# Kernel optimization log

Hardware: AMD Instinct MI355X
Metric: run time of the kernel (lower is better)

The kernel has to match this reference:

```python
import jax, jax.numpy as jnp
from jax import lax
import numpy as np

B, N, C, T = 64, 25, 128, 256
EPS = 1e-5


def setup_inputs() -> dict:
    key = jax.random.key(0)
    ks = jax.random.split(key, 4)
    x = jax.random.normal(ks[0], (B, N, C, T), dtype=jnp.float32)
    adj = jax.random.uniform(ks[1], (N, N), dtype=jnp.float32)
    # row-normalize adjacency like a typical GCN propagation matrix
    adj = adj / jnp.sum(adj, axis=1, keepdims=True)
    # xavier-uniform-ish linear weight [out, in]
    lim = float(np.sqrt(6.0 / (C + C)))
    W_gcn = jax.random.uniform(ks[2], (C, C), minval=-lim, maxval=lim, dtype=jnp.float32)
    b_gcn = jnp.zeros((C,), jnp.float32)
    W_conv = jax.random.normal(ks[3], (C, C, 3), dtype=jnp.float32) * (1.0 / np.sqrt(3 * C))
    b_conv = jnp.zeros((C,), jnp.float32)
    return dict(
        x=x, adj=adj, W_gcn=W_gcn, b_gcn=b_gcn, W_conv=W_conv, b_conv=b_conv,
        tc_gamma=jnp.ones((C,), jnp.float32), tc_beta=jnp.zeros((C,), jnp.float32),
        tc_mean=jnp.zeros((C,), jnp.float32), tc_var=jnp.ones((C,), jnp.float32),
        bn_gamma=jnp.ones((C,), jnp.float32), bn_beta=jnp.zeros((C,), jnp.float32),
        bn_mean=jnp.zeros((C,), jnp.float32), bn_var=jnp.ones((C,), jnp.float32),
    )


def _bn(x, gamma, beta, mean, var, axis):
    # eval-mode batchnorm over channel `axis`
    shape = [1] * x.ndim
    shape[axis] = -1
    g = gamma.reshape(shape)
    b = beta.reshape(shape)
    m = mean.reshape(shape)
    v = var.reshape(shape)
    return g * (x - m) * lax.rsqrt(v + EPS) + b


def reference(x, adj, W_gcn, b_gcn, W_conv, b_conv,
              tc_gamma, tc_beta, tc_mean, tc_var,
              bn_gamma, bn_beta, bn_mean, bn_var):
    # x: [B, N, C, T]; in_channels == out_channels so residual is identity
    b_, n_, c_, t_ = x.shape
    residual = x
    # spatial GCN for all timesteps at once: linear over feature dim, then adj matmul over nodes
    h = jnp.einsum('bnct,oc->bnot', x, W_gcn) + b_gcn[None, None, :, None]
    h = jnp.einsum('mn,bnot->bmot', adj, h)  # [B, N, C, T]
    # temporal conv1d over T for every (batch, node) pair at once
    hc = h.reshape(b_ * n_, c_, t_)
    y = lax.conv_general_dilated(hc, W_conv, window_strides=(1,), padding=[(1, 1)],
                                 dimension_numbers=('NCH', 'OIH', 'NCH'))
    y = y + b_conv[None, :, None]
    y = _bn(y, tc_gamma, tc_beta, tc_mean, tc_var, axis=1)
    y = jax.nn.relu(y)
    y = y.reshape(b_, n_, c_, t_)
    # residual add, block batchnorm over channels, relu
    y = y + residual
    y = _bn(y, bn_gamma, bn_beta, bn_mean, bn_var, axis=2)
    y = jax.nn.relu(y)
    return y
```

## Files before the change

kernel.cpp:

```cpp
#include <hip/hip_runtime.h>
#include <hip/hip_bf16.h>
#include <stdint.h>

#define Bn 64
#define Nn 25
#define Cn 128
#define Tn 256
#define EPSC 1e-5f

typedef short bf16x8 __attribute__((ext_vector_type(8)));
typedef float f32x4 __attribute__((ext_vector_type(4)));
typedef int   i32x4 __attribute__((ext_vector_type(4)));

static constexpr size_t X2T_BYTES  = (size_t)Bn * Nn * Tn * Cn * 2;
static constexpr size_t WEFF_OFF   = X2T_BYTES;
static constexpr size_t WEFF_BYTES = (size_t)3 * 128 * 128 * 2;
static constexpr size_t EPI_OFF    = WEFF_OFF + WEFF_BYTES;
static constexpr size_t ROWSUM_OFF = EPI_OFF + (size_t)7 * 128 * 4;
static constexpr size_t ZPAGE_OFF  = ROWSUM_OFF + 256;
static constexpr size_t WS_NEEDED  = ZPAGE_OFF + 256;

__device__ __forceinline__ uint16_t f2bf(float f) {
    uint32_t u = __builtin_bit_cast(uint32_t, f);
    u = (u + 0x7FFFu + ((u >> 16) & 1u)) >> 16;
    return (uint16_t)u;
}

__device__ __forceinline__ void dma16(const void* gsrc, void* ldst) {
    __builtin_amdgcn_global_load_lds(
        (const __attribute__((address_space(1))) unsigned int*)gsrc,
        (__attribute__((address_space(3))) unsigned int*)ldst, 16, 0, 0);
}

__global__ __launch_bounds__(128) void prep_kernel(
    const float* __restrict__ adj, const float* __restrict__ Wg,
    const float* __restrict__ bg,  const float* __restrict__ Wc,
    const float* __restrict__ bc,
    const float* __restrict__ tg,  const float* __restrict__ tb_,
    const float* __restrict__ tm,  const float* __restrict__ tv,
    const float* __restrict__ bng, const float* __restrict__ bnb,
    const float* __restrict__ bnm, const float* __restrict__ bnv,
    uint16_t* __restrict__ weff, float* __restrict__ epi, float* __restrict__ rowsum,
    uint32_t* __restrict__ zpage)
{
    int blk = blockIdx.x;
    int tid = threadIdx.x;
    if (blk < 384) {
        int k = blk >> 7, o = blk & 127;
        float acc = 0.f;
        for (int i = 0; i < 128; ++i) {
            float wc = Wc[(o * 128 + i) * 3 + k];
            acc = fmaf(wc, Wg[i * 128 + tid], acc);
        }
        weff[((size_t)(k * 128 + o)) * 128 + tid] = f2bf(acc);
    } else {
        int o = tid;
        float b0 = 0.f, b1 = 0.f, b2 = 0.f;
        for (int i = 0; i < 128; ++i) {
            float g = bg[i];
            b0 = fmaf(Wc[(o * 128 + i) * 3 + 0], g, b0);
            b1 = fmaf(Wc[(o * 128 + i) * 3 + 1], g, b1);
            b2 = fmaf(Wc[(o * 128 + i) * 3 + 2], g, b2);
        }
        float a1  = tg[o] * rsqrtf(tv[o] + EPSC);
        float c1p = tb_[o] - a1 * tm[o] + a1 * bc[o];
        float a2  = bng[o] * rsqrtf(bnv[o] + EPSC);
        float c2  = bnb[o] - a2 * bnm[o];
        epi[0 * 128 + o] = a1;
        epi[1 * 128 + o] = c1p;
        epi[2 * 128 + o] = a2;
        epi[3 * 128 + o] = c2;
        epi[4 * 128 + o] = a1 * b0;
        epi[5 * 128 + o] = a1 * b1;
        epi[6 * 128 + o] = a1 * b2;
        if (tid < Nn) {
            float s = 0.f;
            for (int n = 0; n < Nn; ++n) s += adj[tid * Nn + n];
            rowsum[tid] = s;
        }
        if (tid < 64) zpage[tid] = 0u;
    }
}

__global__ __launch_bounds__(256) void adjmix_kernel(
    const float* __restrict__ x, const float* __restrict__ adj,
    uint16_t* __restrict__ x2t)
{
    __shared__ float adjs[Nn * Nn];
    __shared__ float tr[2][2][32][33];

    int bid = blockIdx.x;
    int b  = bid >> 5;
    int rem = bid & 31;
    int cb = rem >> 3, tb = rem & 7;
    int c0 = cb * 32, t0 = tb * 32;
    int tid = threadIdx.x;

    for (int i = tid; i < Nn * Nn; i += 256) adjs[i] = adj[i];
    __syncthreads();

    int cl = tid >> 3;
    int t4 = (tid & 7) * 4;

    float acc[Nn][4];
#pragma unroll
    for (int m = 0; m < Nn; ++m)
#pragma unroll
        for (int j = 0; j < 4; ++j) acc[m][j] = 0.f;

    for (int n = 0; n < Nn; ++n) {
        const float4 v = *reinterpret_cast<const float4*>(
            x + (((size_t)(b * Nn + n) * Cn + c0 + cl) * Tn + t0 + t4));
#pragma unroll
        for (int m = 0; m < Nn; ++m) {
            float a = adjs[m * Nn + n];
            acc[m][0] = fmaf(a, v.x, acc[m][0]);
            acc[m][1] = fmaf(a, v.y, acc[m][1]);
            acc[m][2] = fmaf(a, v.z, acc[m][2]);
            acc[m][3] = fmaf(a, v.w, acc[m][3]);
        }
    }

    int h    = tid & 127;
    int half = tid >> 7;
    int trow = h >> 2;
    int cq   = h & 3;

#pragma unroll
    for (int p = 0; p < 13; ++p) {
        int m0  = 2 * p;
        int buf = p & 1;
#pragma unroll
        for (int j = 0; j < 4; ++j) tr[buf][0][cl][t4 + j] = acc[m0][j];
        if (m0 + 1 < Nn) {
#pragma unroll
            for (int j = 0; j < 4; ++j) tr[buf][1][cl][t4 + j] = acc[m0 + 1][j];
        }
        __syncthreads();
        int mm = m0 + half;
        if (mm < Nn) {
            i32x4 u;
#pragma unroll
            for (int k2 = 0; k2 < 4; ++k2) {
                uint32_t lo16 = f2bf(tr[buf][half][cq * 8 + 2 * k2 + 0][trow]);
                uint32_t hi16 = f2bf(tr[buf][half][cq * 8 + 2 * k2 + 1][trow]);
                u[k2] = (int)(lo16 | (hi16 << 16));
            }
            size_t elem = ((size_t)(b * Nn + mm) * Tn + (t0 + trow)) * Cn + c0 + cq * 8;
            *reinterpret_cast<i32x4*>(x2t + elem) = u;
        }
    }
}

__global__ __launch_bounds__(256, 2) void conv_kernel(
    const uint16_t* __restrict__ x2t, const uint16_t* __restrict__ weff,
    const float* __restrict__ x, const float* __restrict__ epi,
    const float* __restrict__ rowsum, const char* __restrict__ zpage,
    float* __restrict__ out)
{
    constexpr int ROWB = 256;
    constexpr int X2TB = 34 * ROWB;
    constexpr int RESB = 128 * 128;
    constexpr int BUFB = X2TB + RESB;
    __shared__ __align__(16) char ldsb[2 * BUFB];

    int bid = blockIdx.x;
    int m   = bid % Nn;

    int tid = threadIdx.x;
    int w  = tid >> 6;
    int l  = tid & 63;
    int lo = l & 15;
    int hi = l >> 4;
    int o0 = w * 32;

    const char* xp2 = (const char*)x2t + (size_t)bid * Tn * Cn * 2;
    const char* xre = (const char*)x   + (size_t)bid * Cn * Tn * 4;
    const short* wp = (const short*)weff;

    bf16x8 bw[3][4][2];
#pragma unroll
    for (int kk = 0; kk < 3; ++kk)
#pragma unroll
        for (int cc = 0; cc < 4; ++cc)
#pragma unroll
            for (int f = 0; f < 2; ++f) {
                int o = o0 + f * 16 + lo;
                bw[kk][cc][f] = *reinterpret_cast<const bf16x8*>(
                    wp + ((size_t)(kk * 128 + o)) * 128 + cc * 32 + hi * 8);
            }

    float a1[2], c1[2], a2[2], c2v[2], g0[2], g1[2], g2[2];
#pragma unroll
    for (int f = 0; f < 2; ++f) {
        int o = o0 + f * 16 + lo;
        a1[f]  = epi[0 * 128 + o];
        c1[f]  = epi[1 * 128 + o];
        a2[f]  = epi[2 * 128 + o];
        c2v[f] = epi[3 * 128 + o];
        g0[f]  = epi[4 * 128 + o];
        g1[f]  = epi[5 * 128 + o];
        g2[f]  = epi[6 * 128 + o];
    }
    float rs = rowsum[m];
    const size_t obase = (size_t)bid * Cn;

    auto stage = [&](int it, int bufByte) {
        int t0 = it * 32;
#pragma unroll
        for (int oi = 0; oi < 2; ++oi) {
            int rowbase = (w + oi * 4) * 4;
            int r  = rowbase + (l >> 4);
            int cg = l & 15;
            int gt = t0 - 1 + r;
            int sc = cg ^ (r & 7);
            const char* src = (gt >= 0 && gt < Tn)
                ? xp2 + ((size_t)gt * Cn + sc * 8) * 2
                : zpage + sc * 16;
            dma16(src, ldsb + bufByte + rowbase * ROWB);
        }
        if (w == 0 && l < 32) {
            int rowbase = 32;
            int r  = rowbase + (l >> 4);
            int cg = l & 15;
            int gt = t0 - 1 + r;
            int sc = cg ^ (r & 7);
            const char* src = (gt >= 0 && gt < Tn)
                ? xp2 + ((size_t)gt * Cn + sc * 8) * 2
                : zpage + sc * 16;
            dma16(src, ldsb + bufByte + rowbase * ROWB);
        }
#pragma unroll
        for (int oi = 0; oi < 4; ++oi) {
            int p    = w * 4 + oi;
            int orow = p * 8 + (l >> 3);
            int cg   = l & 7;
            int sc   = cg ^ (orow & 7);
            const char* src = xre + (size_t)orow * (Tn * 4) + (size_t)t0 * 4 + sc * 16;
            dma16(src, ldsb + bufByte + X2TB + p * 1024);
        }
    };

    int cur = 0;
    stage(0, 0);
    asm volatile("s_waitcnt vmcnt(0)" ::: "memory");
    __syncthreads();

    for (int it = 0; it < 8; ++it) {
        int nxt = cur ^ 1;
        if (it < 7) stage(it + 1, nxt * BUFB);

        int tq = it * 32;

        f32x4 acc[2][2];
#pragma unroll
        for (int j = 0; j < 2; ++j)
#pragma unroll
            for (int f = 0; f < 2; ++f) acc[j][f] = (f32x4){0.f, 0.f, 0.f, 0.f};

#pragma unroll
        for (int kk = 0; kk < 3; ++kk)
#pragma unroll
            for (int cc = 0; cc < 4; ++cc) {
                bf16x8 af[2];
#pragma unroll
                for (int j = 0; j < 2; ++j) {
                    int lrow  = j * 16 + lo + kk;
                    int lbyte = cur * BUFB + lrow * ROWB +
                                ((cc * 64 + hi * 16) ^ ((lrow & 7) << 4));
                    af[j] = *reinterpret_cast<const bf16x8*>(ldsb + lbyte);
                }
#pragma unroll
                for (int j = 0; j < 2; ++j)
#pragma unroll
                    for (int f = 0; f < 2; ++f)
                        acc[j][f] = __builtin_amdgcn_mfma_f32_16x16x32_bf16(
                            af[j], bw[kk][cc][f], acc[j][f], 0, 0, 0);
            }

#pragma unroll
        for (int j = 0; j < 2; ++j)
#pragma unroll
            for (int f = 0; f < 2; ++f) {
                int o    = o0 + f * 16 + lo;
                int tb4  = tq + j * 16 + hi * 4;
                int rbyte = cur * BUFB + X2TB + o * 128 +
                            ((j * 64 + hi * 16) ^ ((o & 7) << 4));
                f32x4 r4 = *reinterpret_cast<const f32x4*>(ldsb + rbyte);
                f32x4 ov;
#pragma unroll
                for (int qq = 0; qq < 4; ++qq) {
                    int t = tb4 + qq;
                    float gbv = g1[f];
                    if (t > 0)      gbv += g0[f];
                    if (t < Tn - 1) gbv += g2[f];
                    float z = fmaxf(fmaf(a1[f], acc[j][f][qq], fmaf(rs, gbv, c1[f])), 0.f);
                    ov[qq] = fmaxf(fmaf(a2[f], z + r4[qq], c2v[f]), 0.f);
                }
                *reinterpret_cast<f32x4*>(out + (obase + o) * Tn + tb4) = ov;
            }

        asm volatile("s_waitcnt vmcnt(0)" ::: "memory");
        __syncthreads();
        cur = nxt;
    }
}

extern "C" void kernel_launch(void* const* d_in, const int* in_sizes, int n_in,
                              void* d_out, int out_size, void* d_ws, size_t ws_size,
                              hipStream_t stream) {
    const float* x    = (const float*)d_in[0];
    const float* adj  = (const float*)d_in[1];
    const float* Wg   = (const float*)d_in[2];
    const float* bg   = (const float*)d_in[3];
    const float* Wc   = (const float*)d_in[4];
    const float* bc   = (const float*)d_in[5];
    const float* tg   = (const float*)d_in[6];
    const float* tb_  = (const float*)d_in[7];
    const float* tm   = (const float*)d_in[8];
    const float* tv   = (const float*)d_in[9];
    const float* bng  = (const float*)d_in[10];
    const float* bnb  = (const float*)d_in[11];
    const float* bnm  = (const float*)d_in[12];
    const float* bnv  = (const float*)d_in[13];

    if (ws_size < WS_NEEDED) return;

    char* ws = (char*)d_ws;
    uint16_t* x2t    = (uint16_t*)ws;
    uint16_t* weff   = (uint16_t*)(ws + WEFF_OFF);
    float*    epi    = (float*)(ws + EPI_OFF);
    float*    rowsum = (float*)(ws + ROWSUM_OFF);
    char*     zpage  = ws + ZPAGE_OFF;
    float*    out    = (float*)d_out;

    prep_kernel<<<385, 128, 0, stream>>>(adj, Wg, bg, Wc, bc, tg, tb_, tm, tv,
                                         bng, bnb, bnm, bnv, weff, epi, rowsum,
                                         (uint32_t*)zpage);
    adjmix_kernel<<<2048, 256, 0, stream>>>(x, adj, x2t);
    conv_kernel<<<Bn * Nn, 256, 0, stream>>>(x2t, weff, x, epi, rowsum, zpage, out);
}
```

Before: 204.1 us.

## Triple-buffer LDS staging with prefetch distance two and partial vmcnt waits

Moves the conv kernel's LDS staging from double to triple buffering, so tiles are prefetched two iterations ahead. The full `vmcnt(0)` drain before each barrier becomes a partial wait that only requires the older stage's loads. The x2t staging is made uniform at three DMA per thread, with padding rows fed from the zero page, so the vmcnt counts are fixed. The aim is to keep more global loads in flight and hide memory latency behind the MFMA work. In exchange, LDS per block grows to about 75 KB, which could limit occupancy, and the last iterations issue redundant loads.

Measured after the change: 205.5 us. No clear change (+0.7%).

```diff
diff --git a/kernel.cpp b/kernel.cpp
--- a/kernel.cpp
+++ b/kernel.cpp
@@ -159,10 +159,10 @@
     float* __restrict__ out)
 {
     constexpr int ROWB = 256;
-    constexpr int X2TB = 34 * ROWB;
+    constexpr int X2TB = 36 * ROWB;
     constexpr int RESB = 128 * 128;
     constexpr int BUFB = X2TB + RESB;
-    __shared__ __align__(16) char ldsb[2 * BUFB];
+    __shared__ __align__(16) char ldsb[3 * BUFB];
 
     int bid = blockIdx.x;
     int m   = bid % Nn;
@@ -205,27 +205,17 @@
     float rs = rowsum[m];
     const size_t obase = (size_t)bid * Cn;
 
-    auto stage = [&](int it, int bufByte) {
-        int t0 = it * 32;
-#pragma unroll
-        for (int oi = 0; oi < 2; ++oi) {
-            int rowbase = (w + oi * 4) * 4;
+    auto stage = [&](int q, int bufByte) {
+        int t0 = q * 32;
+#pragma unroll
+        for (int oi = 0; oi < 3; ++oi) {
+            int p = w * 3 + oi;
+            int rowbase = p * 4 > 32 ? 32 : p * 4;
             int r  = rowbase + (l >> 4);
             int cg = l & 15;
             int gt = t0 - 1 + r;
             int sc = cg ^ (r & 7);
-            const char* src = (gt >= 0 && gt < Tn)
-                ? xp2 + ((size_t)gt * Cn + sc * 8) * 2
-                : zpage + sc * 16;
-            dma16(src, ldsb + bufByte + rowbase * ROWB);
-        }
-        if (w == 0 && l < 32) {
-            int rowbase = 32;
-            int r  = rowbase + (l >> 4);
-            int cg = l & 15;
-            int gt = t0 - 1 + r;
-            int sc = cg ^ (r & 7);
-            const char* src = (gt >= 0 && gt < Tn)
+            const char* src = (r <= 33 && gt >= 0 && gt < Tn)
                 ? xp2 + ((size_t)gt * Cn + sc * 8) * 2
                 : zpage + sc * 16;
             dma16(src, ldsb + bufByte + rowbase * ROWB);
@@ -241,14 +231,20 @@
         }
     };
 
-    int cur = 0;
     stage(0, 0);
-    asm volatile("s_waitcnt vmcnt(0)" ::: "memory");
-    __syncthreads();
+    stage(1, BUFB);
+    asm volatile("s_waitcnt vmcnt(7)" ::: "memory");
+    __builtin_amdgcn_s_barrier();
+    asm volatile("" ::: "memory");
 
     for (int it = 0; it < 8; ++it) {
-        int nxt = cur ^ 1;
-        if (it < 7) stage(it + 1, nxt * BUFB);
+        int curB = (it % 3) * BUFB;
+
+        {
+            int q = it + 2; if (q > 7) q = 7;
+            stage(q, ((it + 2) % 3) * BUFB);
+        }
+        __builtin_amdgcn_sched_barrier(0);
 
         int tq = it * 32;
 
@@ -266,7 +262,7 @@
 #pragma unroll
                 for (int j = 0; j < 2; ++j) {
                     int lrow  = j * 16 + lo + kk;
-                    int lbyte = cur * BUFB + lrow * ROWB +
+                    int lbyte = curB + lrow * ROWB +
                                 ((cc * 64 + hi * 16) ^ ((lrow & 7) << 4));
                     af[j] = *reinterpret_cast<const bf16x8*>(ldsb + lbyte);
                 }
@@ -284,7 +280,7 @@
             for (int f = 0; f < 2; ++f) {
                 int o    = o0 + f * 16 + lo;
                 int tb4  = tq + j * 16 + hi * 4;
-                int rbyte = cur * BUFB + X2TB + o * 128 +
+                int rbyte = curB + X2TB + o * 128 +
                             ((j * 64 + hi * 16) ^ ((o & 7) << 4));
                 f32x4 r4 = *reinterpret_cast<const f32x4*>(ldsb + rbyte);
                 f32x4 ov;
@@ -300,10 +296,12 @@
                 *reinterpret_cast<f32x4*>(out + (obase + o) * Tn + tb4) = ov;
             }
 
-        asm volatile("s_waitcnt vmcnt(0)" ::: "memory");
-        __syncthreads();
-        cur = nxt;
-    }
+        asm volatile("s_waitcnt vmcnt(11)" ::: "memory");
+        __builtin_amdgcn_s_barrier();
+        asm volatile("" ::: "memory");
+    }
+
+    asm volatile("s_waitcnt vmcnt(0)" ::: "memory");
 }
 
 extern "C" void kernel_launch(void* const* d_in, const int* in_sizes, int n_in,
```
